# Kernel tuning notes

Measured on AMD Instinct MI355X. Metric: run time of the kernel, lower is better.

## Reference

```python
import jax, jax.numpy as jnp
import numpy as np

PI = float(np.pi)


def setup_inputs() -> dict:
    key = jax.random.key(0)
    ks = jax.random.split(key, 12)
    B, S, D, H = 2, 2048, 512, 8
    s = 0.02
    return {
        "q": jax.random.normal(ks[0], (B, S, D), dtype=jnp.float32),
        "k": jax.random.normal(ks[1], (B, S, D), dtype=jnp.float32),
        "v": jax.random.normal(ks[2], (B, S, D), dtype=jnp.float32),
        "xdiff": jax.random.normal(ks[3], (B, S, S), dtype=jnp.float32),
        "Wq": jax.random.normal(ks[4], (D, D), dtype=jnp.float32) * s,
        "bq": jnp.zeros((D,), jnp.float32),
        "Wk": jax.random.normal(ks[5], (D, D), dtype=jnp.float32) * s,
        "bk": jnp.zeros((D,), jnp.float32),
        "Wv": jax.random.normal(ks[6], (D, D), dtype=jnp.float32) * s,
        "bv": jnp.zeros((D,), jnp.float32),
        # 10 stacked Dense(d_model -> num_heads) layers: a,b,c,d,e,f,g,h,i,j
        "Wcoef": jax.random.normal(ks[7], (10, D, H), dtype=jnp.float32) * s,
        "bcoef": jnp.zeros((10, H), jnp.float32),
        "Wo": jax.random.normal(ks[8], (D, D), dtype=jnp.float32) * s,
        "bo": jnp.zeros((D,), jnp.float32),
    }


def reference(q, k, v, xdiff, Wq, bq, Wk, bk, Wv, bv, Wcoef, bcoef, Wo, bo):
    B, S, D = q.shape
    H = Wcoef.shape[-1]
    dh = D // H

    qp = q @ Wq + bq            # (B,S,D)
    kp = k @ Wk + bk
    vp = v @ Wv + bv

    # 10 per-head scalar coefficients computed from the projected queries.
    # coefs: (10, B, H, Sq)
    coefs = jnp.einsum('bsd,ndh->nbhs', qp, Wcoef) + bcoef[:, None, :, None]
    # term 2 uses -0.5*|b|*x^2: abs goes on the coefficient, -0.5 into the basis
    coefs = coefs.at[1].set(jnp.abs(coefs[1]))

    x = xdiff                   # (B, Sq, Sk)
    basis = jnp.stack([
        x,
        -0.5 * x * x,
        jnp.sin(PI * x), jnp.cos(PI * x),
        jnp.sin(3 * PI * x), jnp.cos(3 * PI * x),
        jnp.sin(5 * PI * x), jnp.cos(5 * PI * x),
        jnp.sin(9 * PI * x), jnp.cos(9 * PI * x),
    ])                          # (10, B, Sq, Sk)

    initial_logits = 0.1 * jnp.einsum('nbhq,nbqk->bhqk', coefs, basis)  # (B,H,Sq,Sk)

    qh = qp.reshape(B, S, H, dh).transpose(0, 2, 1, 3)  # (B,H,S,dh)
    kh = kp.reshape(B, S, H, dh).transpose(0, 2, 1, 3)
    vh = vp.reshape(B, S, H, dh).transpose(0, 2, 1, 3)

    logits = (jnp.einsum('bhqd,bhkd->bhqk', qh, kh) + initial_logits) \
             / jnp.sqrt(jnp.asarray(dh, qp.dtype))
    attn = jax.nn.softmax(logits, axis=-1)              # (B,H,Sq,Sk)

    out = jnp.einsum('bhqk,bhkd->bqhd', attn, vh).reshape(B, S, D)
    out = out @ Wo + bo
    return (out, attn)
```

## Files before the change

### kernel.cpp

```cpp
#include <hip/hip_runtime.h>

typedef unsigned short u16;
typedef unsigned int u32;
typedef __attribute__((ext_vector_type(8))) short s16x8;
typedef __attribute__((ext_vector_type(4))) float f32x4;

#define PIf 3.14159265358979323846f

__device__ __forceinline__ float bf2f(u16 u) {
    unsigned v = (unsigned)u << 16;
    return __builtin_bit_cast(float, v);
}
__device__ __forceinline__ u16 f2bf(float f) {
    unsigned u = __builtin_bit_cast(unsigned, f);
    u += 0x7fffu + ((u >> 16) & 1u);
    return (u16)(u >> 16);
}
__device__ __forceinline__ float b2f_lo(unsigned w) { return __builtin_bit_cast(float, w << 16); }
__device__ __forceinline__ float b2f_hi(unsigned w) { return __builtin_bit_cast(float, w & 0xffff0000u); }

#define OFF_FLAG 0
#define OFF_WT   256
#define OFF_WCT  2097408
#define OFF_QB   2179328
#define OFF_KB   6373632
#define OFF_VB   10567936
#define OFF_XB   14762240
#define OFF_QP   31539456
#define OFF_KP   35733760
#define OFF_VP   39928064
#define OFF_VT   44122368
#define OFF_COEF 48316672
#define OFF_CTX  49627392
#define OFF_BIAS 53821696
#define OFF_INV  53829888
#define OFF_PBUF 53960960

__global__ void kdetect(const u32* __restrict__ wq, int* __restrict__ flag) {
    int lane = threadIdx.x;
    float v = fabsf(__builtin_bit_cast(float, wq[lane]));
    bool smallv = (v > 1e-30f) && (v < 0.5f);
    unsigned long long m = __ballot(smallv);
    if (lane == 0) *flag = (__popcll(m) >= 32) ? 1 : 0;
}

__global__ void kcvt3(const void* __restrict__ s0, const void* __restrict__ s1,
                      const void* __restrict__ s2, u16* __restrict__ dst,
                      const int* __restrict__ flag) {
    const void* srcs[3] = {s0, s1, s2};
    const void* src = srcs[blockIdx.y];
    u16* d = dst + (size_t)blockIdx.y * 2097152;
    int i = (blockIdx.x * 256 + threadIdx.x) * 4;
    if (*flag) {
        float4 f = *(const float4*)((const float*)src + i);
        u16 r[4] = {f2bf(f.x), f2bf(f.y), f2bf(f.z), f2bf(f.w)};
        *(uint2*)(d + i) = *(const uint2*)r;
    } else {
        *(uint2*)(d + i) = *(const uint2*)((const u16*)src + i);
    }
}

__global__ void kcvt(const void* __restrict__ src, u16* __restrict__ dst, int n,
                     const int* __restrict__ flag) {
    int i = (blockIdx.x * 256 + threadIdx.x) * 4;
    if (i >= n) return;
    if (*flag) {
        float4 f = *(const float4*)((const float*)src + i);
        u16 r[4] = {f2bf(f.x), f2bf(f.y), f2bf(f.z), f2bf(f.w)};
        *(uint2*)(dst + i) = *(const uint2*)r;
    } else {
        *(uint2*)(dst + i) = *(const uint2*)((const u16*)src + i);
    }
}

__global__ void kbias(const void* __restrict__ bq, const void* __restrict__ bk,
                      const void* __restrict__ bv, const void* __restrict__ bo,
                      const void* __restrict__ bc, u16* __restrict__ dst,
                      const int* __restrict__ flag) {
    int t = threadIdx.x;
    bool f = *flag != 0;
    dst[t]        = f ? f2bf(((const float*)bq)[t]) : ((const u16*)bq)[t];
    dst[512 + t]  = f ? f2bf(((const float*)bk)[t]) : ((const u16*)bk)[t];
    dst[1024 + t] = f ? f2bf(((const float*)bv)[t]) : ((const u16*)bv)[t];
    dst[1536 + t] = f ? f2bf(((const float*)bo)[t]) : ((const u16*)bo)[t];
    if (t < 80)
        dst[2048 + t] = f ? f2bf(((const float*)bc)[t]) : ((const u16*)bc)[t];
}

__global__ void ktrans512(const void* __restrict__ wq, const void* __restrict__ wk,
                          const void* __restrict__ wv, const void* __restrict__ wo,
                          u16* __restrict__ dst, const int* __restrict__ flag) {
    __shared__ u16 t[32][33];
    const void* srcs[4] = {wq, wk, wv, wo};
    const void* src = srcs[blockIdx.z];
    bool f = *flag != 0;
    u16* d = dst + (size_t)blockIdx.z * 512 * 512;
    int x0 = blockIdx.x * 32, y0 = blockIdx.y * 32;
    size_t si = (size_t)(y0 + threadIdx.y) * 512 + x0 + threadIdx.x;
    t[threadIdx.y][threadIdx.x] = f ? f2bf(((const float*)src)[si]) : ((const u16*)src)[si];
    __syncthreads();
    d[(size_t)(x0 + threadIdx.y) * 512 + y0 + threadIdx.x] = t[threadIdx.x][threadIdx.y];
}

__global__ void kwct(const void* __restrict__ wc, u16* __restrict__ dst,
                     const int* __restrict__ flag) {
    int nh = blockIdx.x;
    int n = nh >> 3, h = nh & 7;
    bool f = *flag != 0;
    for (int d = threadIdx.x; d < 512; d += 64) {
        size_t si = ((size_t)n * 512 + d) * 8 + h;
        dst[nh * 512 + d] = f ? f2bf(((const float*)wc)[si]) : ((const u16*)wc)[si];
    }
}

__global__ __launch_bounds__(256) void kgemm(const u16* __restrict__ A, const u16* __restrict__ BT,
                                             const u16* __restrict__ bias, u16* __restrict__ out) {
    __shared__ u16 As[64][40];
    __shared__ u16 Bs[64][40];
    int tid = threadIdx.x;
    int w = tid >> 6, lane = tid & 63, quad = lane >> 4, col = lane & 15;
    int m0 = blockIdx.y * 64, n0 = blockIdx.x * 64;
    int wm = (w >> 1) * 32, wn = (w & 1) * 32;
    int sr = tid >> 2, sc = tid & 3;
    f32x4 acc[2][2] = {};
    for (int kt = 0; kt < 512; kt += 32) {
        __syncthreads();
        *(uint4*)&As[sr][sc * 8] = *(const uint4*)&A[(size_t)(m0 + sr) * 512 + kt + sc * 8];
        *(uint4*)&Bs[sr][sc * 8] = *(const uint4*)&BT[(size_t)(n0 + sr) * 512 + kt + sc * 8];
        __syncthreads();
        s16x8 a[2], b[2];
        a[0] = *(const s16x8*)&As[wm + col][quad * 8];
        a[1] = *(const s16x8*)&As[wm + 16 + col][quad * 8];
        b[0] = *(const s16x8*)&Bs[wn + col][quad * 8];
        b[1] = *(const s16x8*)&Bs[wn + 16 + col][quad * 8];
#pragma unroll
        for (int mi = 0; mi < 2; mi++)
#pragma unroll
            for (int ni = 0; ni < 2; ni++)
                acc[mi][ni] = __builtin_amdgcn_mfma_f32_16x16x32_bf16(a[mi], b[ni], acc[mi][ni], 0, 0, 0);
    }
#pragma unroll
    for (int mi = 0; mi < 2; mi++)
#pragma unroll
        for (int ni = 0; ni < 2; ni++) {
            int n = n0 + wn + ni * 16 + col;
            float bv = bf2f(bias[n]);
#pragma unroll
            for (int r = 0; r < 4; r++) {
                int m = m0 + wm + mi * 16 + quad * 4 + r;
                out[(size_t)m * 512 + n] = f2bf(acc[mi][ni][r] + bv);
            }
        }
}

__global__ __launch_bounds__(256) void kgemm_final(const u16* __restrict__ A, const u16* __restrict__ BT,
                                                   const u16* __restrict__ bias, u16* __restrict__ outH,
                                                   float* __restrict__ outF, const int* __restrict__ flag) {
    bool f32o = *flag != 0;
    __shared__ u16 As[64][40];
    __shared__ u16 Bs[64][40];
    int tid = threadIdx.x;
    int w = tid >> 6, lane = tid & 63, quad = lane >> 4, col = lane & 15;
    int m0 = blockIdx.y * 64, n0 = blockIdx.x * 64;
    int wm = (w >> 1) * 32, wn = (w & 1) * 32;
    int sr = tid >> 2, sc = tid & 3;
    f32x4 acc[2][2] = {};
    for (int kt = 0; kt < 512; kt += 32) {
        __syncthreads();
        *(uint4*)&As[sr][sc * 8] = *(const uint4*)&A[(size_t)(m0 + sr) * 512 + kt + sc * 8];
        *(uint4*)&Bs[sr][sc * 8] = *(const uint4*)&BT[(size_t)(n0 + sr) * 512 + kt + sc * 8];
        __syncthreads();
        s16x8 a[2], b[2];
        a[0] = *(const s16x8*)&As[wm + col][quad * 8];
        a[1] = *(const s16x8*)&As[wm + 16 + col][quad * 8];
        b[0] = *(const s16x8*)&Bs[wn + col][quad * 8];
        b[1] = *(const s16x8*)&Bs[wn + 16 + col][quad * 8];
#pragma unroll
        for (int mi = 0; mi < 2; mi++)
#pragma unroll
            for (int ni = 0; ni < 2; ni++)
                acc[mi][ni] = __builtin_amdgcn_mfma_f32_16x16x32_bf16(a[mi], b[ni], acc[mi][ni], 0, 0, 0);
    }
#pragma unroll
    for (int mi = 0; mi < 2; mi++)
#pragma unroll
        for (int ni = 0; ni < 2; ni++) {
            int n = n0 + wn + ni * 16 + col;
            float bv = bf2f(bias[n]);
#pragma unroll
            for (int r = 0; r < 4; r++) {
                int m = m0 + wm + mi * 16 + quad * 4 + r;
                float val = acc[mi][ni][r] + bv;
                if (f32o) outF[(size_t)m * 512 + n] = val;
                else      outH[(size_t)m * 512 + n] = f2bf(val);
            }
        }
}

__global__ void kvtrans(const u16* __restrict__ vp, u16* __restrict__ vT) {
    __shared__ u16 t[32][33];
    int b = blockIdx.z;
    int d0 = blockIdx.x * 32, s0 = blockIdx.y * 32;
    t[threadIdx.y][threadIdx.x] = vp[((size_t)b * 2048 + s0 + threadIdx.y) * 512 + d0 + threadIdx.x];
    __syncthreads();
    vT[((size_t)b * 512 + d0 + threadIdx.y) * 2048 + s0 + threadIdx.x] = t[threadIdx.x][threadIdx.y];
}

__global__ __launch_bounds__(256) void kcoef(const u16* __restrict__ qp, const u16* __restrict__ wct,
                                             const u16* __restrict__ bc, float* __restrict__ cout) {
    __shared__ u16 As[64][40];
    int tid = threadIdx.x;
    int w = tid >> 6, lane = tid & 63, quad = lane >> 4, col = lane & 15;
    int m0 = blockIdx.x * 64;
    int sr = tid >> 2, sc = tid & 3;
    f32x4 acc[5] = {};
    for (int kt = 0; kt < 512; kt += 32) {
        __syncthreads();
        *(uint4*)&As[sr][sc * 8] = *(const uint4*)&qp[(size_t)(m0 + sr) * 512 + kt + sc * 8];
        __syncthreads();
        s16x8 a = *(const s16x8*)&As[w * 16 + col][quad * 8];
#pragma unroll
        for (int nt = 0; nt < 5; nt++) {
            uint4 bv4 = *(const uint4*)&wct[(size_t)(nt * 16 + col) * 512 + kt + quad * 8];
            acc[nt] = __builtin_amdgcn_mfma_f32_16x16x32_bf16(a, __builtin_bit_cast(s16x8, bv4), acc[nt], 0, 0, 0);
        }
    }
    int m = m0 + w * 16 + quad * 4;
    int b = m >> 11, s = m & 2047;
#pragma unroll
    for (int nt = 0; nt < 5; nt++) {
        int nh = nt * 16 + col, n = nh >> 3, h = nh & 7;
        float bvv = bf2f(bc[nh]);
        float4 o;
        float tmp[4];
#pragma unroll
        for (int r = 0; r < 4; r++) {
            float c = acc[nt][r] + bvv;
            if (n == 1) c = fabsf(c);
            tmp[r] = c * 0.0125f;
        }
        o.x = tmp[0]; o.y = tmp[1]; o.z = tmp[2]; o.w = tmp[3];
        *(float4*)&cout[((size_t)((b * 8 + h) * 10 + n)) * 2048 + s] = o;
    }
}

template <int F32S>
__global__ __launch_bounds__(512) void kattn_t(const u16* __restrict__ qp, const u16* __restrict__ kp,
                                               const u16* __restrict__ vT, const u16* __restrict__ xd,
                                               const float* __restrict__ coef,
                                               u16* __restrict__ attnH, u16* __restrict__ pbuf,
                                               float* __restrict__ p32,
                                               u16* __restrict__ ctx, float* __restrict__ invb,
                                               const int* __restrict__ flag, int big) {
    int fl = *flag;
    if constexpr (F32S) { if (fl != 1) return; }
    else                { if (fl && !big) return; }
    u16* p16 = fl ? pbuf : attnH;

    __shared__ u16 qs[64][72];
    __shared__ u16 ks[128][72];
    __shared__ u16 xs[64][136];
    __shared__ float cfl[10][64];

    int tid = threadIdx.x;
    int lane = tid & 63, quad = lane >> 4, col = lane & 15;
    int w = tid >> 6;
    int wr = w & 3, wc = w >> 2;
    int qt = blockIdx.x, bh = blockIdx.y;
    int b = bh >> 3, h = bh & 7;
    int q0 = qt * 64;

    {
        int r = tid >> 3, qu = tid & 7;
        const u16* src = qp + ((size_t)(b * 2048 + q0 + r)) * 512 + h * 64 + qu * 8;
        *(uint4*)&qs[r][qu * 8] = *(const uint4*)src;
    }
    if (tid < 160) {
        int n = tid >> 4, i = tid & 15;
        *(float4*)&cfl[n][i * 4] = *(const float4*)&coef[((size_t)(bh * 10 + n)) * 2048 + q0 + i * 4];
    }
    __syncthreads();

    float cf[40];
#pragma unroll
    for (int n = 0; n < 10; n++)
#pragma unroll
        for (int r = 0; r < 4; r++) cf[n * 4 + r] = cfl[n][wr * 16 + quad * 4 + r];

    s16x8 a0 = *(const s16x8*)&qs[wr * 16 + col][quad * 8];
    s16x8 a1 = *(const s16x8*)&qs[wr * 16 + col][32 + quad * 8];

    float s_l[4] = {0.f, 0.f, 0.f, 0.f};
    f32x4 accv[4] = {};

    size_t abase = ((size_t)(bh * 2048 + q0)) * 2048;
    const u16* vb0 = vT + ((size_t)(b * 512 + h * 64 + col)) * 2048 + quad * 8;

    for (int k0 = 0; k0 < 2048; k0 += 128) {
        __syncthreads();
        {
            int kr = tid >> 2, hf = tid & 3;
            const u16* src = kp + ((size_t)(b * 2048 + k0 + kr)) * 512 + h * 64 + hf * 16;
            *(uint4*)&ks[kr][hf * 16]     = *(const uint4*)&src[0];
            *(uint4*)&ks[kr][hf * 16 + 8] = *(const uint4*)&src[8];
        }
        {
            int qr = tid >> 3, qu = tid & 7;
            const u16* src = xd + ((size_t)(b * 2048 + q0 + qr)) * 2048 + k0 + qu * 16;
            *(uint4*)&xs[qr][qu * 16]     = *(const uint4*)&src[0];
            *(uint4*)&xs[qr][qu * 16 + 8] = *(const uint4*)&src[8];
        }
        __syncthreads();
#pragma unroll
        for (int nt = 0; nt < 4; nt++) {
            int ntg = wc * 4 + nt;
            s16x8 b0 = *(const s16x8*)&ks[ntg * 16 + col][quad * 8];
            s16x8 b1 = *(const s16x8*)&ks[ntg * 16 + col][32 + quad * 8];
            f32x4 acc = {0.f, 0.f, 0.f, 0.f};
            acc = __builtin_amdgcn_mfma_f32_16x16x32_bf16(a0, b0, acc, 0, 0, 0);
            acc = __builtin_amdgcn_mfma_f32_16x16x32_bf16(a1, b1, acc, 0, 0, 0);
#pragma unroll
            for (int r = 0; r < 4; r++) {
                int lq = wr * 16 + quad * 4 + r;
                int kk = ntg * 16 + col;
                float x = bf2f(xs[lq][kk]);
                float ang = PIf * x;
                float s1 = __sinf(ang), c1 = __cosf(ang);
                float s2 = 2.f * s1 * c1, c2 = 1.f - 2.f * s1 * s1;
                float s3 = s1 * c2 + c1 * s2, c3 = c1 * c2 - s1 * s2;
                float s5 = s3 * c2 + c3 * s2, c5 = c3 * c2 - s3 * s2;
                float s4 = 2.f * s2 * c2, c4 = 1.f - 2.f * s2 * s2;
                float s9 = s5 * c4 + c5 * s4, c9 = c5 * c4 - s5 * s4;
                float dot = cf[0 * 4 + r] * x + cf[1 * 4 + r] * (-0.5f * x * x)
                          + cf[2 * 4 + r] * s1 + cf[3 * 4 + r] * c1
                          + cf[4 * 4 + r] * s3 + cf[5 * 4 + r] * c3
                          + cf[6 * 4 + r] * s5 + cf[7 * 4 + r] * c5
                          + cf[8 * 4 + r] * s9 + cf[9 * 4 + r] * c9;
                float logit = acc[r] * 0.125f + dot;
                float p = __expf(logit);
                size_t idx = abase + (size_t)lq * 2048 + k0 + kk;
                u16 pb = f2bf(p);
                if constexpr (F32S) p32[idx] = p;
                else                p16[idx] = pb;
                s_l[r] += p;
                xs[lq][kk] = pb;
            }
        }
#pragma unroll
        for (int kc2 = 0; kc2 < 2; kc2++) {
            int kc = wc * 2 + kc2;
            s16x8 af = *(const s16x8*)&xs[wr * 16 + col][kc * 32 + quad * 8];
#pragma unroll
            for (int nt = 0; nt < 4; nt++) {
                uint4 bv4 = *(const uint4*)&vb0[(size_t)nt * 16 * 2048 + k0 + kc * 32];
                accv[nt] = __builtin_amdgcn_mfma_f32_16x16x32_bf16(af, __builtin_bit_cast(s16x8, bv4), accv[nt], 0, 0, 0);
            }
        }
    }

    float sred[4];
#pragma unroll
    for (int r = 0; r < 4; r++) {
        float s = s_l[r];
#pragma unroll
        for (int off = 1; off < 16; off <<= 1) s += __shfl_xor(s, off);
        sred[r] = s;
    }

    __syncthreads();
    float* red  = (float*)&ks[0][0];
    float* psum = (float*)&xs[0][0];
    if (wc == 1) {
#pragma unroll
        for (int nt = 0; nt < 4; nt++)
#pragma unroll
            for (int r = 0; r < 4; r++)
                red[(wr * 64 + lane) * 16 + nt * 4 + r] = accv[nt][r];
        if (col == 0) {
#pragma unroll
            for (int r = 0; r < 4; r++) psum[wr * 16 + quad * 4 + r] = sred[r];
        }
    }
    __syncthreads();
    if (wc == 0) {
        float inv_r[4];
#pragma unroll
        for (int r = 0; r < 4; r++)
            inv_r[r] = 1.f / (sred[r] + psum[wr * 16 + quad * 4 + r]);
        if (col == 0) {
#pragma unroll
            for (int r = 0; r < 4; r++)
                invb[bh * 2048 + q0 + wr * 16 + quad * 4 + r] = inv_r[r];
        }
#pragma unroll
        for (int nt = 0; nt < 4; nt++)
#pragma unroll
            for (int r = 0; r < 4; r++) {
                float vsum = accv[nt][r] + red[(wr * 64 + lane) * 16 + nt * 4 + r];
                int q = q0 + wr * 16 + quad * 4 + r;
                int d = h * 64 + nt * 16 + col;
                ctx[((size_t)(b * 2048 + q)) * 512 + d] = f2bf(vsum * inv_r[r]);
            }
    }
}

template <int BIG>
__global__ __launch_bounds__(256) void knorm(u16* __restrict__ attnH, const u16* __restrict__ pbuf,
                                             float* __restrict__ attnF,
                                             const float* __restrict__ invb, const int* __restrict__ flag) {
    int fl = *flag;
    int row = blockIdx.x;
    float inv = invb[row];
    size_t base = (size_t)row * 2048 + threadIdx.x * 8;
    if (fl == 0) {
        uint4 vv = *(const uint4*)&attnH[base];
        unsigned a[4] = {vv.x, vv.y, vv.z, vv.w};
#pragma unroll
        for (int i = 0; i < 4; i++) {
            float lo = b2f_lo(a[i]) * inv;
            float hi = b2f_hi(a[i]) * inv;
            a[i] = ((unsigned)f2bf(hi) << 16) | (unsigned)f2bf(lo);
        }
        uint4 o; o.x = a[0]; o.y = a[1]; o.z = a[2]; o.w = a[3];
        *(uint4*)&attnH[base] = o;
    } else if constexpr (BIG) {
        uint4 vv = *(const uint4*)&pbuf[base];
        unsigned a[4] = {vv.x, vv.y, vv.z, vv.w};
        float4 o0, o1;
        o0.x = b2f_lo(a[0]) * inv; o0.y = b2f_hi(a[0]) * inv;
        o0.z = b2f_lo(a[1]) * inv; o0.w = b2f_hi(a[1]) * inv;
        o1.x = b2f_lo(a[2]) * inv; o1.y = b2f_hi(a[2]) * inv;
        o1.z = b2f_lo(a[3]) * inv; o1.w = b2f_hi(a[3]) * inv;
        *(float4*)&attnF[base] = o0;
        *(float4*)&attnF[base + 4] = o1;
    } else {
        float4 v0 = *(const float4*)&attnF[base];
        float4 v1 = *(const float4*)&attnF[base + 4];
        v0.x *= inv; v0.y *= inv; v0.z *= inv; v0.w *= inv;
        v1.x *= inv; v1.y *= inv; v1.z *= inv; v1.w *= inv;
        *(float4*)&attnF[base] = v0;
        *(float4*)&attnF[base + 4] = v1;
    }
}

extern "C" void kernel_launch(void* const* d_in, const int* in_sizes, int n_in,
                              void* d_out, int out_size, void* d_ws, size_t ws_size,
                              hipStream_t stream) {
    const void* q  = d_in[0];
    const void* k  = d_in[1];
    const void* v  = d_in[2];
    const void* xd = d_in[3];
    const void* Wq = d_in[4];
    const void* bq = d_in[5];
    const void* Wk = d_in[6];
    const void* bk = d_in[7];
    const void* Wv = d_in[8];
    const void* bv = d_in[9];
    const void* Wc = d_in[10];
    const void* bc = d_in[11];
    const void* Wo = d_in[12];
    const void* bo = d_in[13];

    char* ws = (char*)d_ws;
    int*   flag = (int*)(ws + OFF_FLAG);
    u16*   WT   = (u16*)(ws + OFF_WT);
    u16*   WcT  = (u16*)(ws + OFF_WCT);
    u16*   qb   = (u16*)(ws + OFF_QB);
    u16*   kb   = (u16*)(ws + OFF_KB);
    u16*   vb   = (u16*)(ws + OFF_VB);
    u16*   xb   = (u16*)(ws + OFF_XB);
    u16*   qp   = (u16*)(ws + OFF_QP);
    u16*   kp   = (u16*)(ws + OFF_KP);
    u16*   vp   = (u16*)(ws + OFF_VP);
    u16*   vT   = (u16*)(ws + OFF_VT);
    float* coef = (float*)(ws + OFF_COEF);
    u16*   ctx  = (u16*)(ws + OFF_CTX);
    u16*   bB   = (u16*)(ws + OFF_BIAS);
    float* invb = (float*)(ws + OFF_INV);
    u16*   pbuf = (u16*)(ws + OFF_PBUF);

    u16*   outH  = (u16*)d_out;
    u16*   attnH = outH + 2097152;
    float* outF  = (float*)d_out;
    float* attnF = outF + 2097152;

    bool big = ws_size >= (size_t)OFF_PBUF + 134217728ull;

    kdetect<<<1, 64, 0, stream>>>((const u32*)Wq, flag);
    kcvt3<<<dim3(2048, 3), 256, 0, stream>>>(q, k, v, qb, flag);
    kcvt<<<8192, 256, 0, stream>>>(xd, xb, 8388608, flag);
    kbias<<<1, 512, 0, stream>>>(bq, bk, bv, bo, bc, bB, flag);
    ktrans512<<<dim3(16, 16, 4), dim3(32, 32), 0, stream>>>(Wq, Wk, Wv, Wo, WT, flag);
    kwct<<<80, 64, 0, stream>>>(Wc, WcT, flag);
    kgemm<<<dim3(8, 64), 256, 0, stream>>>(qb, WT, bB, qp);
    kgemm<<<dim3(8, 64), 256, 0, stream>>>(kb, WT + 262144, bB + 512, kp);
    kgemm<<<dim3(8, 64), 256, 0, stream>>>(vb, WT + 524288, bB + 1024, vp);
    kvtrans<<<dim3(16, 64, 2), dim3(32, 32), 0, stream>>>(vp, vT);
    kcoef<<<64, 256, 0, stream>>>(qp, WcT, bB + 2048, coef);

    kattn_t<0><<<dim3(32, 16), 512, 0, stream>>>(qp, kp, vT, xb, coef, attnH, pbuf, attnF,
                                                 ctx, invb, flag, (int)big);
    if (!big)
        kattn_t<1><<<dim3(32, 16), 512, 0, stream>>>(qp, kp, vT, xb, coef, attnH, pbuf, attnF,
                                                     ctx, invb, flag, 0);

    if (big) knorm<1><<<32768, 256, 0, stream>>>(attnH, pbuf, attnF, invb, flag);
    else     knorm<0><<<32768, 256, 0, stream>>>(attnH, pbuf, attnF, invb, flag);

    kgemm_final<<<dim3(8, 64), 256, 0, stream>>>(ctx, WT + 786432, bB + 1536, outH, outF, flag);
}
```

Before: 637.9 us.

## Batch QKV projections, fuse V transpose, and prefetch K/x tiles in attention

The three Q/K/V projection GEMMs become one batched launch over blockIdx.z. The V path writes its output transposed straight into vT, so the separate transpose kernel goes away. In the attention kernel, the next K and xdiff tiles are loaded into registers while the current tile is computed, giving a software-pipelined register prefetch. Probability stores are now staged through shared memory and written as coalesced vector stores instead of scattered per-element stores. This raises register pressure, and the V-transposed store uses 8-byte writes strided across rows.

```diff
diff --git a/kernel.cpp b/kernel.cpp
--- a/kernel.cpp
+++ b/kernel.cpp
@@ -113,8 +113,13 @@
     }
 }
 
-__global__ __launch_bounds__(256) void kgemm(const u16* __restrict__ A, const u16* __restrict__ BT,
-                                             const u16* __restrict__ bias, u16* __restrict__ out) {
+__global__ __launch_bounds__(256) void kgemm3(const u16* __restrict__ qkv, const u16* __restrict__ WT,
+                                              const u16* __restrict__ bias, u16* __restrict__ qp,
+                                              u16* __restrict__ kpj, u16* __restrict__ vT) {
+    int z = blockIdx.z;
+    const u16* A  = qkv + (size_t)z * 2097152;
+    const u16* BT = WT + (size_t)z * 262144;
+    const u16* bs = bias + z * 512;
     __shared__ u16 As[64][40];
     __shared__ u16 Bs[64][40];
     int tid = threadIdx.x;
@@ -139,18 +144,35 @@
             for (int ni = 0; ni < 2; ni++)
                 acc[mi][ni] = __builtin_amdgcn_mfma_f32_16x16x32_bf16(a[mi], b[ni], acc[mi][ni], 0, 0, 0);
     }
-#pragma unroll
-    for (int mi = 0; mi < 2; mi++)
-#pragma unroll
-        for (int ni = 0; ni < 2; ni++) {
-            int n = n0 + wn + ni * 16 + col;
-            float bv = bf2f(bias[n]);
-#pragma unroll
-            for (int r = 0; r < 4; r++) {
-                int m = m0 + wm + mi * 16 + quad * 4 + r;
-                out[(size_t)m * 512 + n] = f2bf(acc[mi][ni][r] + bv);
-            }
-        }
+    if (z < 2) {
+        u16* out = z ? kpj : qp;
+#pragma unroll
+        for (int mi = 0; mi < 2; mi++)
+#pragma unroll
+            for (int ni = 0; ni < 2; ni++) {
+                int n = n0 + wn + ni * 16 + col;
+                float bv = bf2f(bs[n]);
+#pragma unroll
+                for (int r = 0; r < 4; r++) {
+                    int m = m0 + wm + mi * 16 + quad * 4 + r;
+                    out[(size_t)m * 512 + n] = f2bf(acc[mi][ni][r] + bv);
+                }
+            }
+    } else {
+#pragma unroll
+        for (int mi = 0; mi < 2; mi++)
+#pragma unroll
+            for (int ni = 0; ni < 2; ni++) {
+                int n = n0 + wn + ni * 16 + col;
+                float bv = bf2f(bs[n]);
+                int m = m0 + wm + mi * 16 + quad * 4;
+                int bb = m >> 11, s = m & 2047;
+                u16 pk4[4];
+#pragma unroll
+                for (int r = 0; r < 4; r++) pk4[r] = f2bf(acc[mi][ni][r] + bv);
+                *(uint2*)&vT[((size_t)(bb * 512 + n)) * 2048 + s] = *(const uint2*)pk4;
+            }
+    }
 }
 
 __global__ __launch_bounds__(256) void kgemm_final(const u16* __restrict__ A, const u16* __restrict__ BT,
@@ -197,15 +219,6 @@
         }
 }
 
-__global__ void kvtrans(const u16* __restrict__ vp, u16* __restrict__ vT) {
-    __shared__ u16 t[32][33];
-    int b = blockIdx.z;
-    int d0 = blockIdx.x * 32, s0 = blockIdx.y * 32;
-    t[threadIdx.y][threadIdx.x] = vp[((size_t)b * 2048 + s0 + threadIdx.y) * 512 + d0 + threadIdx.x];
-    __syncthreads();
-    vT[((size_t)b * 512 + d0 + threadIdx.y) * 2048 + s0 + threadIdx.x] = t[threadIdx.x][threadIdx.y];
-}
-
 __global__ __launch_bounds__(256) void kcoef(const u16* __restrict__ qp, const u16* __restrict__ wct,
                                              const u16* __restrict__ bc, float* __restrict__ cout) {
     __shared__ u16 As[64][40];
@@ -270,15 +283,30 @@
     int b = bh >> 3, h = bh & 7;
     int q0 = qt * 64;
 
+    int kr = tid >> 2, hf = tid & 3;
+    int qr = tid >> 3, qu = tid & 7;
+
+    const u16* ksrc0 = kp + ((size_t)(b * 2048 + kr)) * 512 + h * 64 + hf * 16;
+    const u16* xsrc0 = xd + ((size_t)(b * 2048 + q0 + qr)) * 2048 + qu * 16;
+
+    uint4 kg0 = *(const uint4*)&ksrc0[0];
+    uint4 kg1 = *(const uint4*)&ksrc0[8];
+    uint4 xg0 = *(const uint4*)&xsrc0[0];
+    uint4 xg1 = *(const uint4*)&xsrc0[8];
+
     {
-        int r = tid >> 3, qu = tid & 7;
-        const u16* src = qp + ((size_t)(b * 2048 + q0 + r)) * 512 + h * 64 + qu * 8;
-        *(uint4*)&qs[r][qu * 8] = *(const uint4*)src;
+        int r = tid >> 3, c8 = tid & 7;
+        const u16* src = qp + ((size_t)(b * 2048 + q0 + r)) * 512 + h * 64 + c8 * 8;
+        *(uint4*)&qs[r][c8 * 8] = *(const uint4*)src;
     }
     if (tid < 160) {
         int n = tid >> 4, i = tid & 15;
         *(float4*)&cfl[n][i * 4] = *(const float4*)&coef[((size_t)(bh * 10 + n)) * 2048 + q0 + i * 4];
     }
+    *(uint4*)&ks[kr][hf * 16]     = kg0;
+    *(uint4*)&ks[kr][hf * 16 + 8] = kg1;
+    *(uint4*)&xs[qr][qu * 16]     = xg0;
+    *(uint4*)&xs[qr][qu * 16 + 8] = xg1;
     __syncthreads();
 
     float cf[40];
@@ -296,21 +324,16 @@
     size_t abase = ((size_t)(bh * 2048 + q0)) * 2048;
     const u16* vb0 = vT + ((size_t)(b * 512 + h * 64 + col)) * 2048 + quad * 8;
 
-    for (int k0 = 0; k0 < 2048; k0 += 128) {
-        __syncthreads();
-        {
-            int kr = tid >> 2, hf = tid & 3;
-            const u16* src = kp + ((size_t)(b * 2048 + k0 + kr)) * 512 + h * 64 + hf * 16;
-            *(uint4*)&ks[kr][hf * 16]     = *(const uint4*)&src[0];
-            *(uint4*)&ks[kr][hf * 16 + 8] = *(const uint4*)&src[8];
-        }
-        {
-            int qr = tid >> 3, qu = tid & 7;
-            const u16* src = xd + ((size_t)(b * 2048 + q0 + qr)) * 2048 + k0 + qu * 16;
-            *(uint4*)&xs[qr][qu * 16]     = *(const uint4*)&src[0];
-            *(uint4*)&xs[qr][qu * 16 + 8] = *(const uint4*)&src[8];
-        }
-        __syncthreads();
+    for (int c = 0; c < 16; c++) {
+        int k0 = c * 128;
+        if (c < 15) {
+            const u16* ksrc = ksrc0 + (size_t)(k0 + 128) * 512;
+            const u16* xsrc = xsrc0 + k0 + 128;
+            kg0 = *(const uint4*)&ksrc[0];
+            kg1 = *(const uint4*)&ksrc[8];
+            xg0 = *(const uint4*)&xsrc[0];
+            xg1 = *(const uint4*)&xsrc[8];
+        }
 #pragma unroll
         for (int nt = 0; nt < 4; nt++) {
             int ntg = wc * 4 + nt;
@@ -338,12 +361,8 @@
                           + cf[8 * 4 + r] * s9 + cf[9 * 4 + r] * c9;
                 float logit = acc[r] * 0.125f + dot;
                 float p = __expf(logit);
-                size_t idx = abase + (size_t)lq * 2048 + k0 + kk;
-                u16 pb = f2bf(p);
-                if constexpr (F32S) p32[idx] = p;
-                else                p16[idx] = pb;
                 s_l[r] += p;
-                xs[lq][kk] = pb;
+                xs[lq][kk] = f2bf(p);
             }
         }
 #pragma unroll
@@ -356,6 +375,34 @@
                 accv[nt] = __builtin_amdgcn_mfma_f32_16x16x32_bf16(af, __builtin_bit_cast(s16x8, bv4), accv[nt], 0, 0, 0);
             }
         }
+        __syncthreads();
+        {
+            size_t gbase = abase + (size_t)qr * 2048 + k0 + qu * 16;
+            uint4 v0 = *(const uint4*)&xs[qr][qu * 16];
+            uint4 v1 = *(const uint4*)&xs[qr][qu * 16 + 8];
+            if constexpr (F32S) {
+                unsigned aa[8] = {v0.x, v0.y, v0.z, v0.w, v1.x, v1.y, v1.z, v1.w};
+                float* dst = p32 + gbase;
+#pragma unroll
+                for (int j = 0; j < 4; j++) {
+                    float4 o;
+                    o.x = b2f_lo(aa[2 * j]);     o.y = b2f_hi(aa[2 * j]);
+                    o.z = b2f_lo(aa[2 * j + 1]); o.w = b2f_hi(aa[2 * j + 1]);
+                    *(float4*)&dst[j * 4] = o;
+                }
+            } else {
+                u16* dst = p16 + gbase;
+                *(uint4*)&dst[0] = v0;
+                *(uint4*)&dst[8] = v1;
+            }
+        }
+        if (c < 15) {
+            *(uint4*)&ks[kr][hf * 16]     = kg0;
+            *(uint4*)&ks[kr][hf * 16 + 8] = kg1;
+            *(uint4*)&xs[qr][qu * 16]     = xg0;
+            *(uint4*)&xs[qr][qu * 16 + 8] = xg1;
+        }
+        __syncthreads();
     }
 
     float sred[4];
@@ -367,7 +414,6 @@
         sred[r] = s;
     }
 
-    __syncthreads();
     float* red  = (float*)&ks[0][0];
     float* psum = (float*)&xs[0][0];
     if (wc == 1) {
@@ -466,12 +512,9 @@
     u16*   WT   = (u16*)(ws + OFF_WT);
     u16*   WcT  = (u16*)(ws + OFF_WCT);
     u16*   qb   = (u16*)(ws + OFF_QB);
-    u16*   kb   = (u16*)(ws + OFF_KB);
-    u16*   vb   = (u16*)(ws + OFF_VB);
     u16*   xb   = (u16*)(ws + OFF_XB);
     u16*   qp   = (u16*)(ws + OFF_QP);
     u16*   kp   = (u16*)(ws + OFF_KP);
-    u16*   vp   = (u16*)(ws + OFF_VP);
     u16*   vT   = (u16*)(ws + OFF_VT);
     float* coef = (float*)(ws + OFF_COEF);
     u16*   ctx  = (u16*)(ws + OFF_CTX);
@@ -492,10 +535,7 @@
     kbias<<<1, 512, 0, stream>>>(bq, bk, bv, bo, bc, bB, flag);
     ktrans512<<<dim3(16, 16, 4), dim3(32, 32), 0, stream>>>(Wq, Wk, Wv, Wo, WT, flag);
     kwct<<<80, 64, 0, stream>>>(Wc, WcT, flag);
-    kgemm<<<dim3(8, 64), 256, 0, stream>>>(qb, WT, bB, qp);
-    kgemm<<<dim3(8, 64), 256, 0, stream>>>(kb, WT + 262144, bB + 512, kp);
-    kgemm<<<dim3(8, 64), 256, 0, stream>>>(vb, WT + 524288, bB + 1024, vp);
-    kvtrans<<<dim3(16, 64, 2), dim3(32, 32), 0, stream>>>(vp, vT);
+    kgemm3<<<dim3(8, 64, 3), 256, 0, stream>>>(qb, WT, bB, qp, kp, vT);
     kcoef<<<64, 256, 0, stream>>>(qp, WcT, bB + 2048, coef);
 
     kattn_t<0><<<dim3(32, 16), 512, 0, stream>>>(qp, kp, vT, xb, coef, attnH, pbuf, attnF,
```

Result: faster. 619.8 us (-2.8%).
